# Performance work log

Measured on AMD Instinct MI355X. Metric: run time of the kernel, lower is better.

## Reference

```python
import jax, jax.numpy as jnp
import numpy as np


def _gcn_smooth(X, src, dst, d_inv_sqrt, n):
    """Symmetric-normalized GCN smoothing: D^-1/2 (A + I) D^-1/2 X,
    with undirected edges given as (src, dst) pairs (applied both ways)."""
    norm = d_inv_sqrt[src] * d_inv_sqrt[dst]            # [E]
    out = jax.ops.segment_sum(X[src] * norm[:, None], dst, num_segments=n)
    out = out + jax.ops.segment_sum(X[dst] * norm[:, None], src, num_segments=n)
    out = out + X * (d_inv_sqrt * d_inv_sqrt)[:, None]  # self loops
    return out


def setup_inputs() -> dict:
    key = jax.random.key(0)
    k1, k2, k3, k4, k5 = jax.random.split(key, 5)
    N, E, C_in, C_hid, C_out = 50000, 800000, 128, 64, 40
    X = jax.random.normal(k1, (N, C_in), dtype=jnp.float32)
    edge_index = jax.random.randint(k2, (2, E), 0, N, dtype=jnp.int32)
    s1 = 1.0 / np.sqrt(C_in)
    s2 = 1.0 / np.sqrt(C_hid)
    W1 = jax.random.uniform(k3, (C_in, C_hid), jnp.float32, -s1, s1)
    b1 = jax.random.uniform(k4, (C_hid,), jnp.float32, -s1, s1)
    W2 = jax.random.uniform(k5, (C_hid, C_out), jnp.float32, -s2, s2)
    b2 = jax.random.uniform(jax.random.fold_in(key, 7), (C_out,), jnp.float32, -s2, s2)
    return {"X": X, "W1": W1, "b1": b1, "W2": W2, "b2": b2, "edge_index": edge_index}


def reference(X, W1, b1, W2, b2, edge_index):
    n = X.shape[0]
    src, dst = edge_index[0], edge_index[1]
    ones = jnp.ones(src.shape[0], dtype=X.dtype)
    deg = (1.0
           + jax.ops.segment_sum(ones, dst, num_segments=n)
           + jax.ops.segment_sum(ones, src, num_segments=n))  # deg of A + I
    d_inv_sqrt = jax.lax.rsqrt(deg)

    # Layer 1: theta -> smoothing -> relu (dropout is identity in eval)
    h = X @ W1 + b1
    h = _gcn_smooth(h, src, dst, d_inv_sqrt, n)
    out1 = jax.nn.relu(h)

    # Layer 2 (is_last): theta -> smoothing
    h2 = out1 @ W2 + b2
    out2 = _gcn_smooth(h2, src, dst, d_inv_sqrt, n)
    return (out1, out2)
```

## Files before the change

### kernel.cpp

```cpp
#include <hip/hip_runtime.h>


#define B1 256
#define BT 1024
#define GROWS 512
#define BUCK_SHIFT 6
#define MAXBUCK 4096
#define CAP 4096
#define RCAP 8192
#define WK 136
#define WK2 72

typedef float f32x4 __attribute__((ext_vector_type(4)));
typedef short bf16x8 __attribute__((ext_vector_type(8)));

union Frag { unsigned int u[4]; bf16x8 v; };

__device__ __forceinline__ unsigned int cvt_pk_bf16(float a, float b) {
    unsigned int r;
    asm("v_cvt_pk_bf16_f32 %0, %1, %2" : "=v"(r) : "v"(a), "v"(b));
    return r;
}

__device__ __forceinline__ float bf_lo(unsigned int u) {
    return __uint_as_float(u << 16);
}
__device__ __forceinline__ float bf_hi(unsigned int u) {
    return __uint_as_float(u & 0xffff0000u);
}

__device__ __forceinline__ bf16x8 ld_frag(const unsigned short* p) {
    uint4 t = *reinterpret_cast<const uint4*>(p);
    Frag f; f.u[0] = t.x; f.u[1] = t.y; f.u[2] = t.z; f.u[3] = t.w;
    return f.v;
}

__device__ __forceinline__ void make_frags(const float4 a, const float4 b,
                                           bf16x8& hi8, bf16x8& lo8) {
    Frag hi, lo;
    hi.u[0] = cvt_pk_bf16(a.x, a.y);
    hi.u[1] = cvt_pk_bf16(a.z, a.w);
    hi.u[2] = cvt_pk_bf16(b.x, b.y);
    hi.u[3] = cvt_pk_bf16(b.z, b.w);
    lo.u[0] = cvt_pk_bf16(a.x - __uint_as_float(hi.u[0] << 16),
                          a.y - __uint_as_float(hi.u[0] & 0xffff0000u));
    lo.u[1] = cvt_pk_bf16(a.z - __uint_as_float(hi.u[1] << 16),
                          a.w - __uint_as_float(hi.u[1] & 0xffff0000u));
    lo.u[2] = cvt_pk_bf16(b.x - __uint_as_float(hi.u[2] << 16),
                          b.y - __uint_as_float(hi.u[2] & 0xffff0000u));
    lo.u[3] = cvt_pk_bf16(b.z - __uint_as_float(hi.u[3] << 16),
                          b.w - __uint_as_float(hi.u[3] & 0xffff0000u));
    hi8 = hi.v; lo8 = lo.v;
}

__global__ __launch_bounds__(BT) void k_build_gemm1(
        const int* __restrict__ src, const int* __restrict__ dst,
        int* __restrict__ cursors, unsigned int* __restrict__ binned,
        const float* __restrict__ X, const float* __restrict__ W1,
        const float* __restrict__ b1, unsigned short* __restrict__ hub,
        int E, int nbuck, int chunk, int N) {
    __shared__ __align__(16) char smem[34816];

    if (blockIdx.x < B1) {
        int* lh    = (int*)smem;
        int* lbase = lh + MAXBUCK;
        for (int i = threadIdx.x; i < nbuck; i += BT) lh[i] = 0;
        __syncthreads();
        int e0 = blockIdx.x * chunk;
        int e1 = min(e0 + chunk, E);
        for (int e = e0 + threadIdx.x; e < e1; e += BT) {
            atomicAdd(&lh[src[e] >> BUCK_SHIFT], 1);
            atomicAdd(&lh[dst[e] >> BUCK_SHIFT], 1);
        }
        __syncthreads();
        for (int i = threadIdx.x; i < nbuck; i += BT) {
            int c = lh[i];
            int rel = (c > 0) ? atomicAdd(&cursors[i], c) : 0;
            lbase[i] = i * CAP + rel;
            lh[i] = 0;
        }
        __syncthreads();
        for (int e = e0 + threadIdx.x; e < e1; e += BT) {
            unsigned int s = (unsigned int)src[e];
            unsigned int d = (unsigned int)dst[e];
            int bs = s >> BUCK_SHIFT, bd = d >> BUCK_SHIFT;
            int p = lbase[bs] + atomicAdd(&lh[bs], 1);
            if (p < ((bs + 1) << 12)) binned[p] = (s << 16) | d;
            int q = lbase[bd] + atomicAdd(&lh[bd], 1);
            if (q < ((bd + 1) << 12)) binned[q] = (d << 16) | s;
        }
        return;
    }

    unsigned short* sWhi = (unsigned short*)smem;
    unsigned short* sWlo = sWhi + 64 * WK;
    for (int i = threadIdx.x; i < 128 * 64; i += BT) {
        int c = i >> 7;
        int k = i & 127;
        float w = W1[(size_t)k * 64 + c];
        unsigned int hb = cvt_pk_bf16(w, 0.0f) & 0xffffu;
        float hf = __uint_as_float(hb << 16);
        unsigned int lb = cvt_pk_bf16(w - hf, 0.0f) & 0xffffu;
        sWhi[c * WK + k] = (unsigned short)hb;
        sWlo[c * WK + k] = (unsigned short)lb;
    }
    __syncthreads();

    const int lane = threadIdx.x & 63;
    const int wid  = threadIdx.x >> 6;
    const int ridx = lane & 15;
    const int kgrp = lane >> 4;
    const int r0 = (blockIdx.x - B1) * GROWS + wid * 32;

    f32x4 acc[2][4] = {};

    #pragma unroll
    for (int ks = 0; ks < 4; ++ks) {
        const int ka = ks * 32 + kgrp * 8;
        int ra0 = min(r0 + ridx, N - 1);
        int ra1 = min(r0 + 16 + ridx, N - 1);
        const float4* pa0 = (const float4*)(X + (size_t)ra0 * 128 + ka);
        const float4* pa1 = (const float4*)(X + (size_t)ra1 * 128 + ka);
        float4 a0a = pa0[0], a0b = pa0[1];
        float4 a1a = pa1[0], a1b = pa1[1];
        bf16x8 a0hi, a0lo, a1hi, a1lo;
        make_frags(a0a, a0b, a0hi, a0lo);
        make_frags(a1a, a1b, a1hi, a1lo);
        #pragma unroll
        for (int ct = 0; ct < 4; ++ct) {
            const int cbase = (ct * 16 + ridx) * WK + ka;
            bf16x8 bh = ld_frag(sWhi + cbase);
            bf16x8 bl = ld_frag(sWlo + cbase);
            acc[0][ct] = __builtin_amdgcn_mfma_f32_16x16x32_bf16(a0hi, bh, acc[0][ct], 0, 0, 0);
            acc[0][ct] = __builtin_amdgcn_mfma_f32_16x16x32_bf16(a0lo, bh, acc[0][ct], 0, 0, 0);
            acc[0][ct] = __builtin_amdgcn_mfma_f32_16x16x32_bf16(a0hi, bl, acc[0][ct], 0, 0, 0);
            acc[1][ct] = __builtin_amdgcn_mfma_f32_16x16x32_bf16(a1hi, bh, acc[1][ct], 0, 0, 0);
            acc[1][ct] = __builtin_amdgcn_mfma_f32_16x16x32_bf16(a1lo, bh, acc[1][ct], 0, 0, 0);
            acc[1][ct] = __builtin_amdgcn_mfma_f32_16x16x32_bf16(a1hi, bl, acc[1][ct], 0, 0, 0);
        }
    }

    float bias[4];
    #pragma unroll
    for (int ct = 0; ct < 4; ++ct) bias[ct] = b1[ct * 16 + ridx];

    #pragma unroll
    for (int rt = 0; rt < 2; ++rt) {
        int rb = r0 + rt * 16 + kgrp * 4;
        #pragma unroll
        for (int reg = 0; reg < 4; ++reg) {
            int r = rb + reg;
            if (r < N) {
                #pragma unroll
                for (int ct = 0; ct < 4; ++ct) {
                    float v = acc[rt][ct][reg] + bias[ct];
                    hub[(size_t)r * 64 + ct * 16 + ridx] =
                        (unsigned short)(cvt_pk_bf16(v, 0.0f) & 0xffffu);
                }
            }
        }
    }
}

__global__ __launch_bounds__(256) void k_reorder(const unsigned int* __restrict__ binned,
                                                 const int* __restrict__ cursors,
                                                 unsigned short* __restrict__ adj,
                                                 int* __restrict__ offs,
                                                 int* __restrict__ ends,
                                                 float* __restrict__ dis,
                                                 int N, int nbuck) {
    __shared__ int cnt[64];
    __shared__ int cur[64];
    __shared__ unsigned short stage[RCAP];
    int b = blockIdx.x;
    int start = b * CAP;
    int fill = cursors[b]; if (fill > CAP) fill = CAP;
    int end = start + fill;
    int len = fill;
    if (threadIdx.x < 64) cnt[threadIdx.x] = 0;
    __syncthreads();
    for (int i = start + threadIdx.x; i < end; i += 256)
        atomicAdd(&cnt[(binned[i] >> 16) & 63], 1);
    __syncthreads();
    if (threadIdx.x == 0) {
        int run = 0;
        for (int l = 0; l < 64; ++l) { cur[l] = run; run += cnt[l]; }
    }
    __syncthreads();
    if (threadIdx.x < 64) {
        int node = (b << BUCK_SHIFT) + threadIdx.x;
        if (node < N) {
            int o = start + cur[threadIdx.x];
            offs[node] = o;
            ends[node] = o + cnt[threadIdx.x];
            dis[node]  = rsqrtf(1.0f + (float)cnt[threadIdx.x]);
        }
    }
    __syncthreads();
    if (len <= RCAP) {
        for (int i = start + threadIdx.x; i < end; i += 256) {
            unsigned int v = binned[i];
            int nl = (v >> 16) & 63;
            int p = atomicAdd(&cur[nl], 1);
            stage[p] = (unsigned short)(v & 0xffffu);
        }
        __syncthreads();
        for (int i = threadIdx.x; i < len; i += 256)
            adj[start + i] = stage[i];
    } else {
        for (int i = start + threadIdx.x; i < end; i += 256) {
            unsigned int v = binned[i];
            int nl = (v >> 16) & 63;
            int p = atomicAdd(&cur[nl], 1);
            adj[start + p] = (unsigned short)(v & 0xffffu);
        }
    }
}

__global__ __launch_bounds__(256) void k_gather64(const unsigned int* __restrict__ hsu,
                                                  const unsigned short* __restrict__ adj,
                                                  const int* __restrict__ offs,
                                                  const int* __restrict__ ends,
                                                  const float* __restrict__ dis,
                                                  float* __restrict__ out1, int N) {
    int node = (blockIdx.x * 256 + threadIdx.x) >> 6;
    if (node >= N) return;
    int lane = threadIdx.x & 63;
    int half = lane >> 5;
    int c2 = lane & 31;
    int k   = offs[node];
    int end = ends[node];
    float acc0 = 0.f, acc1 = 0.f;
    for (; k + 16 <= end; k += 16) {
        int j0 = adj[k +  0 + half], j1 = adj[k +  2 + half];
        int j2 = adj[k +  4 + half], j3 = adj[k +  6 + half];
        int j4 = adj[k +  8 + half], j5 = adj[k + 10 + half];
        int j6 = adj[k + 12 + half], j7 = adj[k + 14 + half];
        float d0 = dis[j0], d1 = dis[j1], d2 = dis[j2], d3 = dis[j3];
        float d4 = dis[j4], d5 = dis[j5], d6 = dis[j6], d7 = dis[j7];
        unsigned int u0 = hsu[(size_t)j0 * 32 + c2];
        unsigned int u1 = hsu[(size_t)j1 * 32 + c2];
        unsigned int u2 = hsu[(size_t)j2 * 32 + c2];
        unsigned int u3 = hsu[(size_t)j3 * 32 + c2];
        unsigned int u4 = hsu[(size_t)j4 * 32 + c2];
        unsigned int u5 = hsu[(size_t)j5 * 32 + c2];
        unsigned int u6 = hsu[(size_t)j6 * 32 + c2];
        unsigned int u7 = hsu[(size_t)j7 * 32 + c2];
        acc0 = fmaf(d0, bf_lo(u0), acc0); acc1 = fmaf(d0, bf_hi(u0), acc1);
        acc0 = fmaf(d1, bf_lo(u1), acc0); acc1 = fmaf(d1, bf_hi(u1), acc1);
        acc0 = fmaf(d2, bf_lo(u2), acc0); acc1 = fmaf(d2, bf_hi(u2), acc1);
        acc0 = fmaf(d3, bf_lo(u3), acc0); acc1 = fmaf(d3, bf_hi(u3), acc1);
        acc0 = fmaf(d4, bf_lo(u4), acc0); acc1 = fmaf(d4, bf_hi(u4), acc1);
        acc0 = fmaf(d5, bf_lo(u5), acc0); acc1 = fmaf(d5, bf_hi(u5), acc1);
        acc0 = fmaf(d6, bf_lo(u6), acc0); acc1 = fmaf(d6, bf_hi(u6), acc1);
        acc0 = fmaf(d7, bf_lo(u7), acc0); acc1 = fmaf(d7, bf_hi(u7), acc1);
    }
    for (; k + 8 <= end; k += 8) {
        int j0 = adj[k + 0 + half], j1 = adj[k + 2 + half];
        int j2 = adj[k + 4 + half], j3 = adj[k + 6 + half];
        float d0 = dis[j0], d1 = dis[j1], d2 = dis[j2], d3 = dis[j3];
        unsigned int u0 = hsu[(size_t)j0 * 32 + c2];
        unsigned int u1 = hsu[(size_t)j1 * 32 + c2];
        unsigned int u2 = hsu[(size_t)j2 * 32 + c2];
        unsigned int u3 = hsu[(size_t)j3 * 32 + c2];
        acc0 = fmaf(d0, bf_lo(u0), acc0); acc1 = fmaf(d0, bf_hi(u0), acc1);
        acc0 = fmaf(d1, bf_lo(u1), acc0); acc1 = fmaf(d1, bf_hi(u1), acc1);
        acc0 = fmaf(d2, bf_lo(u2), acc0); acc1 = fmaf(d2, bf_hi(u2), acc1);
        acc0 = fmaf(d3, bf_lo(u3), acc0); acc1 = fmaf(d3, bf_hi(u3), acc1);
    }
    for (; k + 2 <= end; k += 2) {
        int j = adj[k + half];
        float d = dis[j];
        unsigned int u = hsu[(size_t)j * 32 + c2];
        acc0 = fmaf(d, bf_lo(u), acc0);
        acc1 = fmaf(d, bf_hi(u), acc1);
    }
    if (k < end && half == 0) {
        int j = adj[k];
        float d = dis[j];
        unsigned int u = hsu[(size_t)j * 32 + c2];
        acc0 = fmaf(d, bf_lo(u), acc0);
        acc1 = fmaf(d, bf_hi(u), acc1);
    }
    acc0 += __shfl_xor(acc0, 32);
    acc1 += __shfl_xor(acc1, 32);
    float d = dis[node];
    unsigned int us = hsu[(size_t)node * 32 + c2];
    acc0 = fmaf(d, bf_lo(us), acc0);
    acc1 = fmaf(d, bf_hi(us), acc1);
    if (half == 0) {
        float2 r;
        r.x = fmaxf(d * acc0, 0.0f);
        r.y = fmaxf(d * acc1, 0.0f);
        *reinterpret_cast<float2*>(out1 + (size_t)node * 64 + 2 * c2) = r;
    }
}

__global__ __launch_bounds__(256) void k_gemm2_mfma(const float* __restrict__ A,
                                                    const float* __restrict__ W2,
                                                    const float* __restrict__ b2,
                                                    const float* __restrict__ dis,
                                                    unsigned short* __restrict__ h2sb,
                                                    int N) {
    __shared__ unsigned short sWhi[48 * WK2];
    __shared__ unsigned short sWlo[48 * WK2];
    for (int i = threadIdx.x; i < 48 * 64; i += 256) {
        int c = i >> 6;
        int k = i & 63;
        float w = (c < 40) ? W2[(size_t)k * 40 + c] : 0.0f;
        unsigned int hb = cvt_pk_bf16(w, 0.0f) & 0xffffu;
        float hf = __uint_as_float(hb << 16);
        unsigned int lb = cvt_pk_bf16(w - hf, 0.0f) & 0xffffu;
        sWhi[c * WK2 + k] = (unsigned short)hb;
        sWlo[c * WK2 + k] = (unsigned short)lb;
    }
    __syncthreads();

    const int lane = threadIdx.x & 63;
    const int wid  = threadIdx.x >> 6;
    const int ridx = lane & 15;
    const int kgrp = lane >> 4;
    const int r0 = blockIdx.x * 128 + wid * 32;
    if (r0 >= N) return;

    f32x4 acc[2][3] = {};

    #pragma unroll
    for (int ks = 0; ks < 2; ++ks) {
        const int ka = ks * 32 + kgrp * 8;
        int ra0 = min(r0 + ridx, N - 1);
        int ra1 = min(r0 + 16 + ridx, N - 1);
        const float4* pa0 = (const float4*)(A + (size_t)ra0 * 64 + ka);
        const float4* pa1 = (const float4*)(A + (size_t)ra1 * 64 + ka);
        float4 a0a = pa0[0], a0b = pa0[1];
        float4 a1a = pa1[0], a1b = pa1[1];
        bf16x8 a0hi, a0lo, a1hi, a1lo;
        make_frags(a0a, a0b, a0hi, a0lo);
        make_frags(a1a, a1b, a1hi, a1lo);
        #pragma unroll
        for (int ct = 0; ct < 3; ++ct) {
            const int cbase = (ct * 16 + ridx) * WK2 + ka;
            bf16x8 bh = ld_frag(sWhi + cbase);
            bf16x8 bl = ld_frag(sWlo + cbase);
            acc[0][ct] = __builtin_amdgcn_mfma_f32_16x16x32_bf16(a0hi, bh, acc[0][ct], 0, 0, 0);
            acc[0][ct] = __builtin_amdgcn_mfma_f32_16x16x32_bf16(a0lo, bh, acc[0][ct], 0, 0, 0);
            acc[0][ct] = __builtin_amdgcn_mfma_f32_16x16x32_bf16(a0hi, bl, acc[0][ct], 0, 0, 0);
            acc[1][ct] = __builtin_amdgcn_mfma_f32_16x16x32_bf16(a1hi, bh, acc[1][ct], 0, 0, 0);
            acc[1][ct] = __builtin_amdgcn_mfma_f32_16x16x32_bf16(a1lo, bh, acc[1][ct], 0, 0, 0);
            acc[1][ct] = __builtin_amdgcn_mfma_f32_16x16x32_bf16(a1hi, bl, acc[1][ct], 0, 0, 0);
        }
    }

    float bias[3];
    #pragma unroll
    for (int ct = 0; ct < 3; ++ct) {
        int c = ct * 16 + ridx;
        bias[ct] = (c < 40) ? b2[c] : 0.0f;
    }

    #pragma unroll
    for (int rt = 0; rt < 2; ++rt) {
        int rb = r0 + rt * 16 + kgrp * 4;
        #pragma unroll
        for (int reg = 0; reg < 4; ++reg) {
            int r = rb + reg;
            if (r < N) {
                float dv = dis[r];
                #pragma unroll
                for (int ct = 0; ct < 3; ++ct) {
                    int c = ct * 16 + ridx;
                    if (c < 40) {
                        float v = (acc[rt][ct][reg] + bias[ct]) * dv;
                        h2sb[(size_t)r * 40 + c] =
                            (unsigned short)(cvt_pk_bf16(v, 0.0f) & 0xffffu);
                    }
                }
            }
        }
    }
}

__global__ __launch_bounds__(256) void k_gather40(const unsigned int* __restrict__ h2u,
                                                  const unsigned short* __restrict__ adj,
                                                  const int* __restrict__ offs,
                                                  const int* __restrict__ ends,
                                                  const float* __restrict__ dis,
                                                  float* __restrict__ out, int N) {
    int node = (blockIdx.x * 256 + threadIdx.x) >> 6;
    if (node >= N) return;
    int lane = threadIdx.x & 63;
    int half = lane >> 5;
    int c2 = lane & 31;
    bool act = c2 < 20;
    int k   = offs[node];
    int end = ends[node];
    float acc0 = 0.f, acc1 = 0.f;
    for (; k + 8 <= end; k += 8) {
        int j0 = adj[k + 0 + half];
        int j1 = adj[k + 2 + half];
        int j2 = adj[k + 4 + half];
        int j3 = adj[k + 6 + half];
        if (act) {
            unsigned int u0 = h2u[(size_t)j0 * 20 + c2];
            unsigned int u1 = h2u[(size_t)j1 * 20 + c2];
            unsigned int u2 = h2u[(size_t)j2 * 20 + c2];
            unsigned int u3 = h2u[(size_t)j3 * 20 + c2];
            acc0 += (bf_lo(u0) + bf_lo(u1)) + (bf_lo(u2) + bf_lo(u3));
            acc1 += (bf_hi(u0) + bf_hi(u1)) + (bf_hi(u2) + bf_hi(u3));
        }
    }
    for (; k + 2 <= end; k += 2) {
        int j = adj[k + half];
        if (act) {
            unsigned int u = h2u[(size_t)j * 20 + c2];
            acc0 += bf_lo(u);
            acc1 += bf_hi(u);
        }
    }
    if (k < end && half == 0 && act) {
        int j = adj[k];
        unsigned int u = h2u[(size_t)j * 20 + c2];
        acc0 += bf_lo(u);
        acc1 += bf_hi(u);
    }
    acc0 += __shfl_xor(acc0, 32);
    acc1 += __shfl_xor(acc1, 32);
    if (half == 0 && act) {
        unsigned int us = h2u[(size_t)node * 20 + c2];
        float d = dis[node];
        float2 r;
        r.x = d * (acc0 + bf_lo(us));
        r.y = d * (acc1 + bf_hi(us));
        *reinterpret_cast<float2*>(out + (size_t)node * 40 + 2 * c2) = r;
    }
}

extern "C" void kernel_launch(void* const* d_in, const int* in_sizes, int n_in,
                              void* d_out, int out_size, void* d_ws, size_t ws_size,
                              hipStream_t stream) {
    const float* X  = (const float*)d_in[0];
    const float* W1 = (const float*)d_in[1];
    const float* b1 = (const float*)d_in[2];
    const float* W2 = (const float*)d_in[3];
    const float* b2 = (const float*)d_in[4];
    const int*   ei = (const int*)d_in[5];

    const int Chid = in_sizes[2];
    const int Cin  = in_sizes[1] / Chid;
    const int N    = in_sizes[0] / Cin;
    const int E    = in_sizes[5] / 2;

    const int* src = ei;
    const int* dst = ei + E;

    const int nbuck = (N + 63) >> BUCK_SHIFT;
    const int chunk = (E + B1 - 1) / B1;
    const size_t slots = (size_t)nbuck * CAP;

    auto align256 = [](size_t x) { return (x + 255) & ~(size_t)255; };
    char* p = (char*)d_ws;
    int*   cursors = (int*)p; p += align256((size_t)nbuck * 4);
    float* dis     = (float*)p; p += align256((size_t)N * 4);
    int*   offs    = (int*)p; p += align256((size_t)N * 4);
    int*   ends    = (int*)p; p += align256((size_t)N * 4);
    unsigned short* adj = (unsigned short*)p; p += align256(slots * 2);
    unsigned int* binned = (unsigned int*)p; p += align256(slots * 4);
    unsigned int* h2u    = binned;
    unsigned short* hub  = (unsigned short*)p;

    float* out1 = (float*)d_out;
    float* out2 = out1 + (size_t)N * 64;

    hipMemsetAsync(cursors, 0, (size_t)nbuck * 4, stream);

    const int gemmBlocks = (N + GROWS - 1) / GROWS;
    k_build_gemm1<<<B1 + gemmBlocks, BT, 0, stream>>>(src, dst, cursors, binned,
                                                      X, W1, b1, hub,
                                                      E, nbuck, chunk, N);
    k_reorder<<<nbuck, 256, 0, stream>>>(binned, cursors, adj, offs, ends, dis,
                                         N, nbuck);
    k_gather64<<<(N + 3) / 4, 256, 0, stream>>>((const unsigned int*)hub, adj,
                                                offs, ends, dis, out1, N);
    k_gemm2_mfma<<<(N + 127) / 128, 256, 0, stream>>>(out1, W2, b2, dis,
                                                      (unsigned short*)h2u, N);
    k_gather40<<<(N + 3) / 4, 256, 0, stream>>>(h2u, adj, offs, ends, dis, out2, N);
}
```

Baseline: 124.3 us.

## Cache edges in registers across binning passes and use 3-way lane split in gather40

The bucket-binning pass now keeps the first four edge pairs per thread in registers, so the scatter pass does not reload src/dst. The reorder kernel holds up to 16 binned entries per thread in registers, always stages through shared memory sized to CAP, and drops the fallback path that wrote directly to global. The 40-channel gather now splits each wavefront into three 20-lane groups instead of two, so 60 of 64 lanes are busy rather than 40, and combines the partial sums with two shuffles. Costs are extra register pressure and a less regular loop tail.

```diff
diff --git a/kernel.cpp b/kernel.cpp
--- a/kernel.cpp
+++ b/kernel.cpp
@@ -7,7 +7,6 @@
 #define BUCK_SHIFT 6
 #define MAXBUCK 4096
 #define CAP 4096
-#define RCAP 8192
 #define WK 136
 #define WK2 72
 
@@ -68,7 +67,18 @@
         __syncthreads();
         int e0 = blockIdx.x * chunk;
         int e1 = min(e0 + chunk, E);
-        for (int e = e0 + threadIdx.x; e < e1; e += BT) {
+        int es[4], eds[4];
+        #pragma unroll
+        for (int i = 0; i < 4; ++i) {
+            int e = e0 + threadIdx.x + i * BT;
+            if (e < e1) {
+                int s = src[e], d = dst[e];
+                es[i] = s; eds[i] = d;
+                atomicAdd(&lh[s >> BUCK_SHIFT], 1);
+                atomicAdd(&lh[d >> BUCK_SHIFT], 1);
+            }
+        }
+        for (int e = e0 + threadIdx.x + 4 * BT; e < e1; e += BT) {
             atomicAdd(&lh[src[e] >> BUCK_SHIFT], 1);
             atomicAdd(&lh[dst[e] >> BUCK_SHIFT], 1);
         }
@@ -80,7 +90,20 @@
             lh[i] = 0;
         }
         __syncthreads();
-        for (int e = e0 + threadIdx.x; e < e1; e += BT) {
+        #pragma unroll
+        for (int i = 0; i < 4; ++i) {
+            int e = e0 + threadIdx.x + i * BT;
+            if (e < e1) {
+                unsigned int s = (unsigned int)es[i];
+                unsigned int d = (unsigned int)eds[i];
+                int bs = s >> BUCK_SHIFT, bd = d >> BUCK_SHIFT;
+                int p = lbase[bs] + atomicAdd(&lh[bs], 1);
+                if (p < ((bs + 1) << 12)) binned[p] = (s << 16) | d;
+                int q = lbase[bd] + atomicAdd(&lh[bd], 1);
+                if (q < ((bd + 1) << 12)) binned[q] = (d << 16) | s;
+            }
+        }
+        for (int e = e0 + threadIdx.x + 4 * BT; e < e1; e += BT) {
             unsigned int s = (unsigned int)src[e];
             unsigned int d = (unsigned int)dst[e];
             int bs = s >> BUCK_SHIFT, bd = d >> BUCK_SHIFT;
@@ -171,16 +194,23 @@
                                                  int N, int nbuck) {
     __shared__ int cnt[64];
     __shared__ int cur[64];
-    __shared__ unsigned short stage[RCAP];
+    __shared__ unsigned short stage[CAP];
     int b = blockIdx.x;
     int start = b * CAP;
     int fill = cursors[b]; if (fill > CAP) fill = CAP;
     int end = start + fill;
-    int len = fill;
     if (threadIdx.x < 64) cnt[threadIdx.x] = 0;
     __syncthreads();
-    for (int i = start + threadIdx.x; i < end; i += 256)
-        atomicAdd(&cnt[(binned[i] >> 16) & 63], 1);
+    unsigned int vv[16];
+    #pragma unroll
+    for (int i = 0; i < 16; ++i) {
+        int idx = start + threadIdx.x + i * 256;
+        if (idx < end) {
+            unsigned int v = binned[idx];
+            vv[i] = v;
+            atomicAdd(&cnt[(v >> 16) & 63], 1);
+        }
+    }
     __syncthreads();
     if (threadIdx.x == 0) {
         int run = 0;
@@ -197,24 +227,19 @@
         }
     }
     __syncthreads();
-    if (len <= RCAP) {
-        for (int i = start + threadIdx.x; i < end; i += 256) {
-            unsigned int v = binned[i];
+    #pragma unroll
+    for (int i = 0; i < 16; ++i) {
+        int idx = start + threadIdx.x + i * 256;
+        if (idx < end) {
+            unsigned int v = vv[i];
             int nl = (v >> 16) & 63;
             int p = atomicAdd(&cur[nl], 1);
             stage[p] = (unsigned short)(v & 0xffffu);
         }
-        __syncthreads();
-        for (int i = threadIdx.x; i < len; i += 256)
-            adj[start + i] = stage[i];
-    } else {
-        for (int i = start + threadIdx.x; i < end; i += 256) {
-            unsigned int v = binned[i];
-            int nl = (v >> 16) & 63;
-            int p = atomicAdd(&cur[nl], 1);
-            adj[start + p] = (unsigned short)(v & 0xffffu);
-        }
-    }
+    }
+    __syncthreads();
+    for (int i = threadIdx.x; i < fill; i += 256)
+        adj[start + i] = stage[i];
 }
 
 __global__ __launch_bounds__(256) void k_gather64(const unsigned int* __restrict__ hsu,
@@ -389,49 +414,46 @@
     int node = (blockIdx.x * 256 + threadIdx.x) >> 6;
     if (node >= N) return;
     int lane = threadIdx.x & 63;
-    int half = lane >> 5;
-    int c2 = lane & 31;
-    bool act = c2 < 20;
+    int g = lane / 20;
+    int c = lane - g * 20;
+    bool act = g < 3;
     int k   = offs[node];
     int end = ends[node];
     float acc0 = 0.f, acc1 = 0.f;
-    for (; k + 8 <= end; k += 8) {
-        int j0 = adj[k + 0 + half];
-        int j1 = adj[k + 2 + half];
-        int j2 = adj[k + 4 + half];
-        int j3 = adj[k + 6 + half];
+    for (; k + 6 <= end; k += 6) {
         if (act) {
-            unsigned int u0 = h2u[(size_t)j0 * 20 + c2];
-            unsigned int u1 = h2u[(size_t)j1 * 20 + c2];
-            unsigned int u2 = h2u[(size_t)j2 * 20 + c2];
-            unsigned int u3 = h2u[(size_t)j3 * 20 + c2];
-            acc0 += (bf_lo(u0) + bf_lo(u1)) + (bf_lo(u2) + bf_lo(u3));
-            acc1 += (bf_hi(u0) + bf_hi(u1)) + (bf_hi(u2) + bf_hi(u3));
-        }
-    }
-    for (; k + 2 <= end; k += 2) {
-        int j = adj[k + half];
+            int ja = adj[k + g];
+            int jb = adj[k + 3 + g];
+            unsigned int ua = h2u[(size_t)ja * 20 + c];
+            unsigned int ub = h2u[(size_t)jb * 20 + c];
+            acc0 += bf_lo(ua) + bf_lo(ub);
+            acc1 += bf_hi(ua) + bf_hi(ub);
+        }
+    }
+    for (; k + 3 <= end; k += 3) {
         if (act) {
-            unsigned int u = h2u[(size_t)j * 20 + c2];
+            int j = adj[k + g];
+            unsigned int u = h2u[(size_t)j * 20 + c];
             acc0 += bf_lo(u);
             acc1 += bf_hi(u);
         }
     }
-    if (k < end && half == 0 && act) {
-        int j = adj[k];
-        unsigned int u = h2u[(size_t)j * 20 + c2];
+    int rem = end - k;
+    if (act && g < rem) {
+        int j = adj[k + g];
+        unsigned int u = h2u[(size_t)j * 20 + c];
         acc0 += bf_lo(u);
         acc1 += bf_hi(u);
     }
-    acc0 += __shfl_xor(acc0, 32);
-    acc1 += __shfl_xor(acc1, 32);
-    if (half == 0 && act) {
-        unsigned int us = h2u[(size_t)node * 20 + c2];
+    acc0 += __shfl(acc0, lane + 20) + __shfl(acc0, lane + 40);
+    acc1 += __shfl(acc1, lane + 20) + __shfl(acc1, lane + 40);
+    if (lane < 20) {
+        unsigned int us = h2u[(size_t)node * 20 + c];
         float d = dis[node];
         float2 r;
         r.x = d * (acc0 + bf_lo(us));
         r.y = d * (acc1 + bf_hi(us));
-        *reinterpret_cast<float2*>(out + (size_t)node * 40 + 2 * c2) = r;
+        *reinterpret_cast<float2*>(out + (size_t)node * 40 + 2 * c) = r;
     }
 }
 
```

Result: no change. 124.7 us (+0.4%).
